# Kernel optimization log

Hardware: AMD Instinct MI355X
Metric: run time of the kernel (lower is better)

## Reference

```python
import jax, jax.numpy as jnp
import numpy as np

EMBED_DIM = 768
NUM_HEADS = 12
HEAD_DIM = EMBED_DIM // NUM_HEADS


def setup_inputs() -> dict:
    key = jax.random.key(0)
    ks = jax.random.split(key, 9)
    B, N, D = 8, 1024, EMBED_DIM
    s = 1.0 / np.sqrt(D)
    x = jax.random.normal(ks[0], (B, N, D), dtype=jnp.float32)
    Wq = jax.random.normal(ks[1], (D, D), dtype=jnp.float32) * s
    bq = jnp.zeros((D,), dtype=jnp.float32)
    Wk = jax.random.normal(ks[2], (D, D), dtype=jnp.float32) * s
    bk = jnp.zeros((D,), dtype=jnp.float32)
    Wv = jax.random.normal(ks[3], (D, D), dtype=jnp.float32) * s
    bv = jnp.zeros((D,), dtype=jnp.float32)
    Wo = jax.random.normal(ks[4], (D, D), dtype=jnp.float32) * s
    bo = jnp.zeros((D,), dtype=jnp.float32)
    return {"x": x, "Wq": Wq, "bq": bq, "Wk": Wk, "bk": bk,
            "Wv": Wv, "bv": bv, "Wo": Wo, "bo": bo}


def reference(x, Wq, bq, Wk, bk, Wv, bv, Wo, bo):
    B, N, D = x.shape
    H, Hd = NUM_HEADS, HEAD_DIM
    # torch Linear: y = x @ W.T + b
    q = (x @ Wq.T + bq).reshape(B, N, H, Hd).transpose(0, 2, 1, 3)  # [B,H,N,Hd]
    k = (x @ Wk.T + bk).reshape(B, N, H, Hd).transpose(0, 2, 1, 3)
    v = (x @ Wv.T + bv).reshape(B, N, H, Hd).transpose(0, 2, 1, 3)
    # NOTE: original scales by embed_dim**-0.5 (not head_dim)
    scale = jnp.asarray(D, x.dtype) ** -0.5
    scores = jnp.einsum('bhnd,bhmd->bhnm', q, k) * scale  # [B,H,N,N]
    attn = jax.nn.softmax(scores, axis=-1)
    out = jnp.einsum('bhnm,bhmd->bhnd', attn, v)  # dropout: identity in eval
    out = out.transpose(0, 2, 1, 3).reshape(B, N, D)
    return out @ Wo.T + bo
```

## Files before the change

### kernel.cpp

```cpp
#include <hip/hip_runtime.h>
#include <math.h>


typedef __bf16 bf16x8 __attribute__((ext_vector_type(8)));
typedef float  f32x4  __attribute__((ext_vector_type(4)));
typedef unsigned u32x2 __attribute__((ext_vector_type(2)));
typedef unsigned u32x4 __attribute__((ext_vector_type(4)));
typedef unsigned short ushort_t;

__device__ __forceinline__ unsigned short f2bf(float f) {
    unsigned u = __float_as_uint(f);
    u += 0x7fffu + ((u >> 16) & 1u);
    return (unsigned short)(u >> 16);
}
__device__ __forceinline__ unsigned pk16(unsigned short lo, unsigned short hi) {
    return (unsigned)lo | ((unsigned)hi << 16);
}

#define GLL16(g, l)                                                                        \
    __builtin_amdgcn_global_load_lds((const __attribute__((address_space(1))) void*)(g),   \
                                     (__attribute__((address_space(3))) void*)(l), 16, 0, 0)

__global__ __launch_bounds__(256)
void cast_all(const float* __restrict__ x,
              const float* __restrict__ w0, const float* __restrict__ w1,
              const float* __restrict__ w2, const float* __restrict__ w3,
              ushort_t* __restrict__ xb, ushort_t* __restrict__ wb0,
              ushort_t* __restrict__ wb1, ushort_t* __restrict__ wb2,
              ushort_t* __restrict__ wb3)
{
    const int y = blockIdx.y;
    const float* s; ushort_t* d; int n;
    switch (y) {
        case 0:  s = x;  d = xb;  n = 8192 * 768; break;
        case 1:  s = w0; d = wb0; n = 768 * 768;  break;
        case 2:  s = w1; d = wb1; n = 768 * 768;  break;
        case 3:  s = w2; d = wb2; n = 768 * 768;  break;
        default: s = w3; d = wb3; n = 768 * 768;  break;
    }
    const int i = (blockIdx.x * 256 + threadIdx.x) * 8;
    if (i >= n) return;
    const float4 f0 = *(const float4*)(s + i);
    const float4 f1 = *(const float4*)(s + i + 4);
    ushort4 p0, p1;
    p0.x = f2bf(f0.x); p0.y = f2bf(f0.y); p0.z = f2bf(f0.z); p0.w = f2bf(f0.w);
    p1.x = f2bf(f1.x); p1.y = f2bf(f1.y); p1.z = f2bf(f1.z); p1.w = f2bf(f1.w);
    *(ushort4*)(d + i)     = p0;
    *(ushort4*)(d + i + 4) = p1;
}

__device__ __forceinline__ void gemm_core_mfma(
    const ushort_t* __restrict__ A, const ushort_t* __restrict__ W,
    int m0, int n0, ushort_t* smem, f32x4 acc[4][4])
{
    ushort_t* As = smem;
    ushort_t* Ws = smem + 4096;
    const int tid = threadIdx.x;
    const int L   = tid & 63;
    const int wv  = tid >> 6;
    const int wr  = wv >> 1, wc = wv & 1;
    const int c   = L & 15,  g  = L >> 4;

    const int c0 = tid, c1 = tid + 256;
    const int qs = ((tid & 3) ^ ((tid >> 3) & 3)) * 8;
    const ushort_t* a0 = A + (size_t)(m0 + (c0 >> 2)) * 768 + qs;
    const ushort_t* a1 = A + (size_t)(m0 + (c1 >> 2)) * 768 + qs;
    const ushort_t* w0 = W + (size_t)(n0 + (c0 >> 2)) * 768 + qs;
    const ushort_t* w1 = W + (size_t)(n0 + (c1 >> 2)) * 768 + qs;
    const int sg = (g ^ ((c >> 1) & 3)) * 8;

#pragma unroll
    for (int i = 0; i < 4; ++i)
#pragma unroll
        for (int j = 0; j < 4; ++j) acc[i][j] = (f32x4){0.f, 0.f, 0.f, 0.f};

    for (int k0 = 0; k0 < 768; k0 += 32) {
        __syncthreads();
        GLL16(a0 + k0, &As[(size_t)c0 * 8]);
        GLL16(a1 + k0, &As[(size_t)c1 * 8]);
        GLL16(w0 + k0, &Ws[(size_t)c0 * 8]);
        GLL16(w1 + k0, &Ws[(size_t)c1 * 8]);
        __syncthreads();
        bf16x8 af[4], bfr[4];
#pragma unroll
        for (int i = 0; i < 4; ++i)
            af[i] = *(const bf16x8*)&As[(wr * 64 + i * 16 + c) * 32 + sg];
#pragma unroll
        for (int j = 0; j < 4; ++j)
            bfr[j] = *(const bf16x8*)&Ws[(wc * 64 + j * 16 + c) * 32 + sg];
#pragma unroll
        for (int i = 0; i < 4; ++i)
#pragma unroll
            for (int j = 0; j < 4; ++j)
                acc[i][j] = __builtin_amdgcn_mfma_f32_16x16x32_bf16(
                    af[i], bfr[j], acc[i][j], 0, 0, 0);
    }
}

__global__ __launch_bounds__(256, 3)
void gemm_qkv(const ushort_t* __restrict__ xb,
              const ushort_t* __restrict__ wqb, const ushort_t* __restrict__ wkb,
              const ushort_t* __restrict__ wvb,
              const float* __restrict__ bq, const float* __restrict__ bk,
              const float* __restrict__ bv,
              ushort_t* __restrict__ Qh, ushort_t* __restrict__ Kl,
              ushort_t* __restrict__ Vl)
{
    __shared__ ushort_t smem[8192];
    const int z = blockIdx.z;
    const ushort_t* W   = (z == 0) ? wqb : (z == 1) ? wkb : wvb;
    const float*    bia = (z == 0) ? bq  : (z == 1) ? bk  : bv;
    const int m0 = blockIdx.y * 128, n0 = blockIdx.x * 128;
    f32x4 acc[4][4];
    gemm_core_mfma(xb, W, m0, n0, smem, acc);

    const int tid = threadIdx.x, L = tid & 63, wv2 = tid >> 6;
    const int wr = wv2 >> 1, wc = wv2 & 1, c = L & 15, g = L >> 4;
    ushort_t* scr = smem + wv2 * 1280;
    const int h = (n0 + wc * 64) >> 6;
    float bsv[4];
#pragma unroll
    for (int j = 0; j < 4; ++j) bsv[j] = bia[n0 + wc * 64 + j * 16 + c];

    __syncthreads();
#pragma unroll
    for (int i = 0; i < 4; ++i) {
        const int rowg = m0 + wr * 64 + i * 16;
        const int b  = rowg >> 10;
        const int nb = rowg & 1023;
        const int bh = b * 12 + h;
        if (z < 2) {
#pragma unroll
            for (int j = 0; j < 4; ++j)
#pragma unroll
                for (int r = 0; r < 4; ++r)
                    scr[(g * 4 + r) * 72 + j * 16 + c] = f2bf(acc[i][j][r] + bsv[j]);
            if (z == 0) {
                const int row = L >> 2, qp = L & 3;
                const u32x4 v0 = *(const u32x4*)&scr[row * 72 + qp * 16];
                const u32x4 v1 = *(const u32x4*)&scr[row * 72 + qp * 16 + 8];
                ushort_t* dst = Qh + ((size_t)bh * 1024 + nb + row) * 64 + qp * 16;
                *(u32x4*)dst       = v0;
                *(u32x4*)(dst + 8) = v1;
            } else {
                const int n16 = L >> 2, q1 = L & 3;
                const u32x4 va  = *(const u32x4*)&scr[n16 * 72 + q1 * 8];
                const u32x4 vb2 = *(const u32x4*)&scr[n16 * 72 + q1 * 8 + 32];
                ushort_t* base = Kl + (size_t)bh * 65536 + (size_t)(nb >> 4) * 1024;
                *(u32x4*)&base[q1 * 128 + n16 * 8]       = va;
                *(u32x4*)&base[512 + q1 * 128 + n16 * 8] = vb2;
            }
        } else {
#pragma unroll
            for (int j = 0; j < 4; ++j) {
                const unsigned w01 = pk16(f2bf(acc[i][j][0] + bsv[j]),
                                          f2bf(acc[i][j][1] + bsv[j]));
                const unsigned w23 = pk16(f2bf(acc[i][j][2] + bsv[j]),
                                          f2bf(acc[i][j][3] + bsv[j]));
                const int a = (j * 16 + c) * 20 + g * 4;
                *(unsigned*)&scr[a]     = w01;
                *(unsigned*)&scr[a + 2] = w23;
            }
            const u32x2 r0 = *(const u32x2*)&scr[L * 20];
            const u32x2 r1 = *(const u32x2*)&scr[L * 20 + 4];
            const u32x2 r2 = *(const u32x2*)&scr[L * 20 + 8];
            const u32x2 r3 = *(const u32x2*)&scr[L * 20 + 12];
            const int ht = L >> 4, cV = L & 15;
            const int T = nb >> 6, u = (nb >> 5) & 1, gVa = (nb >> 3) & 3;
            ushort_t* vb = Vl + (((size_t)(bh * 4 + ht) * 16 + T) * 2 + u) * 512 + cV * 8;
            *(u32x4*)&vb[gVa * 128]       = (u32x4){r0.x, r0.y, r1.x, r1.y};
            *(u32x4*)&vb[(gVa + 1) * 128] = (u32x4){r2.x, r2.y, r3.x, r3.y};
        }
    }
}

__global__ __launch_bounds__(256, 3)
void gemm_outp(const ushort_t* __restrict__ attnb, const ushort_t* __restrict__ wob,
               const float* __restrict__ bo, float* __restrict__ out)
{
    __shared__ ushort_t smem[8192];
    const int m0 = blockIdx.y * 128, n0 = blockIdx.x * 128;
    f32x4 acc[4][4];
    gemm_core_mfma(attnb, wob, m0, n0, smem, acc);
    const int tid = threadIdx.x, L = tid & 63, wv2 = tid >> 6;
    const int wr = wv2 >> 1, wc = wv2 & 1, c = L & 15, g = L >> 4;
#pragma unroll
    for (int i = 0; i < 4; ++i) {
        const int row = m0 + wr * 64 + i * 16 + g * 4;
#pragma unroll
        for (int j = 0; j < 4; ++j) {
            const int col = n0 + wc * 64 + j * 16 + c;
            const float bsvo = bo[col];
#pragma unroll
            for (int r = 0; r < 4; ++r)
                out[(size_t)(row + r) * 768 + col] = acc[i][j][r] + bsvo;
        }
    }
}

__global__ __launch_bounds__(64, 3)
void flash_bf16(const ushort_t* __restrict__ Q, const ushort_t* __restrict__ Kl,
                const ushort_t* __restrict__ Vl, ushort_t* __restrict__ attnb)
{
    __shared__ ushort_t Ps[2][16 * 68];
    const int L = threadIdx.x;
    const int c = L & 15, g = L >> 4;
    const int bh = blockIdx.x, q0 = blockIdx.y * 32;
    const float SC2 = 0.05205954985329743f;

    const ushort_t* Qp = Q + ((size_t)bh * 1024 + q0 + c) * 64 + g * 8;
    bf16x8 qf[2][2];
    qf[0][0] = *(const bf16x8*)Qp;
    qf[0][1] = *(const bf16x8*)(Qp + 32);
    qf[1][0] = *(const bf16x8*)(Qp + 16 * 64);
    qf[1][1] = *(const bf16x8*)(Qp + 16 * 64 + 32);

    const ushort_t* Kb = Kl + (size_t)bh * 65536 + (size_t)L * 8;
    const ushort_t* Vb = Vl + (size_t)bh * 65536 + (size_t)L * 8;

    f32x4 o[2][4];
#pragma unroll
    for (int w = 0; w < 2; ++w)
#pragma unroll
        for (int ht = 0; ht < 4; ++ht) o[w][ht] = (f32x4){0.f, 0.f, 0.f, 0.f};
    float ls[2] = {0.f, 0.f};

    bf16x8 kf0[4], kf1[4];
#pragma unroll
    for (int ct = 0; ct < 4; ++ct) {
        kf0[ct] = *(const bf16x8*)(Kb + (size_t)(ct * 2 + 0) * 512);
        kf1[ct] = *(const bf16x8*)(Kb + (size_t)(ct * 2 + 1) * 512);
    }

    for (int T = 0; T < 16; ++T) {
        bf16x8 vf0[4], vf1[4];
#pragma unroll
        for (int ht = 0; ht < 4; ++ht) {
            const ushort_t* vp = Vb + (size_t)((ht * 16 + T) * 2) * 512;
            vf0[ht] = *(const bf16x8*)vp;
            vf1[ht] = *(const bf16x8*)(vp + 512);
        }
        f32x4 s[2][4];
#pragma unroll
        for (int w = 0; w < 2; ++w)
#pragma unroll
            for (int ct = 0; ct < 4; ++ct) {
                f32x4 zz = (f32x4){0.f, 0.f, 0.f, 0.f};
                zz = __builtin_amdgcn_mfma_f32_16x16x32_bf16(kf0[ct], qf[w][0], zz, 0, 0, 0);
                zz = __builtin_amdgcn_mfma_f32_16x16x32_bf16(kf1[ct], qf[w][1], zz, 0, 0, 0);
                s[w][ct] = zz;
            }
        const int Tn = (T < 15) ? T + 1 : 15;
#pragma unroll
        for (int ct = 0; ct < 4; ++ct) {
            const ushort_t* kp = Kb + (size_t)((Tn * 4 + ct) * 2) * 512;
            kf0[ct] = *(const bf16x8*)kp;
            kf1[ct] = *(const bf16x8*)(kp + 512);
        }
#pragma unroll
        for (int w = 0; w < 2; ++w) {
#pragma unroll
            for (int ct = 0; ct < 4; ++ct) {
                float p[4];
#pragma unroll
                for (int r = 0; r < 4; ++r)
                    p[r] = __builtin_amdgcn_exp2f(s[w][ct][r] * SC2);
                ls[w] += (p[0] + p[1]) + (p[2] + p[3]);
                const unsigned w01 = __builtin_amdgcn_perm(
                    __float_as_uint(p[1]), __float_as_uint(p[0]), 0x07060302u);
                const unsigned w23 = __builtin_amdgcn_perm(
                    __float_as_uint(p[3]), __float_as_uint(p[2]), 0x07060302u);
                *(u32x2*)&Ps[w][c * 68 + ct * 16 + g * 4] = (u32x2){w01, w23};
            }
        }
#pragma unroll
        for (int w = 0; w < 2; ++w) {
            const int pb = c * 68 + g * 8;
            const u32x4 pa  = *(const u32x4*)&Ps[w][pb];
            const u32x4 pbv = *(const u32x4*)&Ps[w][pb + 32];
            const bf16x8 pf0 = __builtin_bit_cast(bf16x8, pa);
            const bf16x8 pf1 = __builtin_bit_cast(bf16x8, pbv);
#pragma unroll
            for (int ht = 0; ht < 4; ++ht) {
                o[w][ht] = __builtin_amdgcn_mfma_f32_16x16x32_bf16(vf0[ht], pf0, o[w][ht], 0, 0, 0);
                o[w][ht] = __builtin_amdgcn_mfma_f32_16x16x32_bf16(vf1[ht], pf1, o[w][ht], 0, 0, 0);
            }
        }
    }

    const int b = bh / 12, h = bh % 12;
#pragma unroll
    for (int w = 0; w < 2; ++w) {
        float l = ls[w];
        l += __shfl_xor(l, 16);
        l += __shfl_xor(l, 32);
        const float inv = 1.f / l;
#pragma unroll
        for (int ht = 0; ht < 4; ++ht) {
            const unsigned w0 = pk16(f2bf(o[w][ht][0] * inv), f2bf(o[w][ht][1] * inv));
            const unsigned w1 = pk16(f2bf(o[w][ht][2] * inv), f2bf(o[w][ht][3] * inv));
            *(u32x2*)&Ps[w][c * 68 + ht * 16 + g * 4] = (u32x2){w0, w1};
        }
#pragma unroll
        for (int e = 0; e < 2; ++e) {
            const int row = e * 8 + (L >> 3);
            const int ch  = L & 7;
            const int si  = row * 68 + ch * 8;
            const u32x2 t0 = *(const u32x2*)&Ps[w][si];
            const u32x2 t1 = *(const u32x2*)&Ps[w][si + 4];
            *(u32x4*)&attnb[((size_t)(b * 1024 + q0 + w * 16 + row)) * 768 + h * 64 + ch * 8]
                = (u32x4){t0.x, t0.y, t1.x, t1.y};
        }
    }
}

extern "C" void kernel_launch(void* const* d_in, const int* in_sizes, int n_in,
                              void* d_out, int out_size, void* d_ws, size_t ws_size,
                              hipStream_t stream)
{
    const float* x  = (const float*)d_in[0];
    const float* Wq = (const float*)d_in[1];
    const float* bq = (const float*)d_in[2];
    const float* Wk = (const float*)d_in[3];
    const float* bk = (const float*)d_in[4];
    const float* Wv = (const float*)d_in[5];
    const float* bv = (const float*)d_in[6];
    const float* Wo = (const float*)d_in[7];
    const float* bo = (const float*)d_in[8];
    float* out = (float*)d_out;

    char* ws = (char*)d_ws;
    ushort_t* xb    = (ushort_t*)(ws);
    ushort_t* wqb   = (ushort_t*)(ws + 12582912);
    ushort_t* wkb   = (ushort_t*)(ws + 12582912 + 1179648);
    ushort_t* wvb   = (ushort_t*)(ws + 12582912 + 2359296);
    ushort_t* wob   = (ushort_t*)(ws + 12582912 + 3538944);
    ushort_t* Qh    = (ushort_t*)(ws + 17301504);
    ushort_t* Kl    = (ushort_t*)(ws + 29884416);
    ushort_t* Vl    = (ushort_t*)(ws + 42467328);
    ushort_t* attnb = (ushort_t*)(ws + 55050240);

    cast_all<<<dim3(3072, 5), 256, 0, stream>>>(x, Wq, Wk, Wv, Wo,
                                                xb, wqb, wkb, wvb, wob);
    gemm_qkv<<<dim3(6, 64, 3), 256, 0, stream>>>(xb, wqb, wkb, wvb,
                                                 bq, bk, bv, Qh, Kl, Vl);
    flash_bf16<<<dim3(96, 32), 64, 0, stream>>>(Qh, Kl, Vl, attnb);
    gemm_outp<<<dim3(6, 64), 256, 0, stream>>>(attnb, wob, bo, out);
}
```

Before: 198.7 us.

## Fuse Q/K/V projections into one GEMM sharing the x tile across three weights

The QKV projection previously launched a separate grid slice per weight matrix, each reloading the same x tile. It now computes all three projections in one block on a 64x128 tile. The block loads x once per k-step alongside three weight tiles and keeps three accumulator sets. Epilogues are rewritten per output layout for Q, K and V. This cuts redundant x traffic and LDS loads, at the cost of more registers per thread and smaller M tiles, which may reduce occupancy.

```diff
diff --git a/kernel.cpp b/kernel.cpp
--- a/kernel.cpp
+++ b/kernel.cpp
@@ -106,71 +106,125 @@
               ushort_t* __restrict__ Qh, ushort_t* __restrict__ Kl,
               ushort_t* __restrict__ Vl)
 {
-    __shared__ ushort_t smem[8192];
-    const int z = blockIdx.z;
-    const ushort_t* W   = (z == 0) ? wqb : (z == 1) ? wkb : wvb;
-    const float*    bia = (z == 0) ? bq  : (z == 1) ? bk  : bv;
-    const int m0 = blockIdx.y * 128, n0 = blockIdx.x * 128;
-    f32x4 acc[4][4];
-    gemm_core_mfma(xb, W, m0, n0, smem, acc);
-
-    const int tid = threadIdx.x, L = tid & 63, wv2 = tid >> 6;
-    const int wr = wv2 >> 1, wc = wv2 & 1, c = L & 15, g = L >> 4;
-    ushort_t* scr = smem + wv2 * 1280;
-    const int h = (n0 + wc * 64) >> 6;
-    float bsv[4];
-#pragma unroll
-    for (int j = 0; j < 4; ++j) bsv[j] = bia[n0 + wc * 64 + j * 16 + c];
+    __shared__ ushort_t smem[14336];
+    ushort_t* As  = smem;
+    ushort_t* Ws0 = smem + 2048;
+    ushort_t* Ws1 = smem + 6144;
+    ushort_t* Ws2 = smem + 10240;
+
+    const int tid = threadIdx.x, L = tid & 63, wv = tid >> 6;
+    const int c = L & 15, g = L >> 4;
+    const int n0 = blockIdx.x * 128, m0 = blockIdx.y * 64;
+
+    const int qs = ((tid & 3) ^ ((tid >> 3) & 3)) * 8;
+    const ushort_t* ap = xb  + (size_t)(m0 + (tid >> 2)) * 768 + qs;
+    const ushort_t* wq = wqb + (size_t)(n0 + (tid >> 2)) * 768 + qs;
+    const ushort_t* wk = wkb + (size_t)(n0 + (tid >> 2)) * 768 + qs;
+    const ushort_t* wvp = wvb + (size_t)(n0 + (tid >> 2)) * 768 + qs;
+    const size_t st64 = (size_t)64 * 768;
+    const int sg = (g ^ ((c >> 1) & 3)) * 8;
+
+    f32x4 acc[3][4][2];
+#pragma unroll
+    for (int z = 0; z < 3; ++z)
+#pragma unroll
+        for (int i = 0; i < 4; ++i)
+#pragma unroll
+            for (int j = 0; j < 2; ++j) acc[z][i][j] = (f32x4){0.f, 0.f, 0.f, 0.f};
+
+    for (int k0 = 0; k0 < 768; k0 += 32) {
+        __syncthreads();
+        GLL16(ap + k0,          &As[(size_t)tid * 8]);
+        GLL16(wq + k0,          &Ws0[(size_t)tid * 8]);
+        GLL16(wq + st64 + k0,   &Ws0[(size_t)(tid + 256) * 8]);
+        GLL16(wk + k0,          &Ws1[(size_t)tid * 8]);
+        GLL16(wk + st64 + k0,   &Ws1[(size_t)(tid + 256) * 8]);
+        GLL16(wvp + k0,         &Ws2[(size_t)tid * 8]);
+        GLL16(wvp + st64 + k0,  &Ws2[(size_t)(tid + 256) * 8]);
+        __syncthreads();
+        bf16x8 af[4];
+#pragma unroll
+        for (int i = 0; i < 4; ++i)
+            af[i] = *(const bf16x8*)&As[(i * 16 + c) * 32 + sg];
+        bf16x8 bf[3][2];
+        const ushort_t* wsz[3] = {Ws0, Ws1, Ws2};
+#pragma unroll
+        for (int z = 0; z < 3; ++z)
+#pragma unroll
+            for (int j = 0; j < 2; ++j)
+                bf[z][j] = *(const bf16x8*)&wsz[z][(wv * 32 + j * 16 + c) * 32 + sg];
+#pragma unroll
+        for (int z = 0; z < 3; ++z)
+#pragma unroll
+            for (int i = 0; i < 4; ++i)
+#pragma unroll
+                for (int j = 0; j < 2; ++j)
+                    acc[z][i][j] = __builtin_amdgcn_mfma_f32_16x16x32_bf16(
+                        af[i], bf[z][j], acc[z][i][j], 0, 0, 0);
+    }
+
+    const int b  = m0 >> 10, nb = m0 & 1023;
+    const int hcol = n0 + wv * 32;
+    const int h = hcol >> 6, uh = (hcol >> 5) & 1;
+    const int bh = b * 12 + h;
+    ushort_t* scr = smem + wv * 2304;
+
+    float bias2[3][2];
+#pragma unroll
+    for (int j = 0; j < 2; ++j) {
+        bias2[0][j] = bq[hcol + j * 16 + c];
+        bias2[1][j] = bk[hcol + j * 16 + c];
+        bias2[2][j] = bv[hcol + j * 16 + c];
+    }
 
     __syncthreads();
-#pragma unroll
-    for (int i = 0; i < 4; ++i) {
-        const int rowg = m0 + wr * 64 + i * 16;
-        const int b  = rowg >> 10;
-        const int nb = rowg & 1023;
-        const int bh = b * 12 + h;
-        if (z < 2) {
-#pragma unroll
-            for (int j = 0; j < 4; ++j)
-#pragma unroll
-                for (int r = 0; r < 4; ++r)
-                    scr[(g * 4 + r) * 72 + j * 16 + c] = f2bf(acc[i][j][r] + bsv[j]);
-            if (z == 0) {
-                const int row = L >> 2, qp = L & 3;
-                const u32x4 v0 = *(const u32x4*)&scr[row * 72 + qp * 16];
-                const u32x4 v1 = *(const u32x4*)&scr[row * 72 + qp * 16 + 8];
-                ushort_t* dst = Qh + ((size_t)bh * 1024 + nb + row) * 64 + qp * 16;
-                *(u32x4*)dst       = v0;
-                *(u32x4*)(dst + 8) = v1;
-            } else {
-                const int n16 = L >> 2, q1 = L & 3;
-                const u32x4 va  = *(const u32x4*)&scr[n16 * 72 + q1 * 8];
-                const u32x4 vb2 = *(const u32x4*)&scr[n16 * 72 + q1 * 8 + 32];
-                ushort_t* base = Kl + (size_t)bh * 65536 + (size_t)(nb >> 4) * 1024;
-                *(u32x4*)&base[q1 * 128 + n16 * 8]       = va;
-                *(u32x4*)&base[512 + q1 * 128 + n16 * 8] = vb2;
-            }
-        } else {
-#pragma unroll
-            for (int j = 0; j < 4; ++j) {
-                const unsigned w01 = pk16(f2bf(acc[i][j][0] + bsv[j]),
-                                          f2bf(acc[i][j][1] + bsv[j]));
-                const unsigned w23 = pk16(f2bf(acc[i][j][2] + bsv[j]),
-                                          f2bf(acc[i][j][3] + bsv[j]));
-                const int a = (j * 16 + c) * 20 + g * 4;
-                *(unsigned*)&scr[a]     = w01;
-                *(unsigned*)&scr[a + 2] = w23;
-            }
-            const u32x2 r0 = *(const u32x2*)&scr[L * 20];
-            const u32x2 r1 = *(const u32x2*)&scr[L * 20 + 4];
-            const u32x2 r2 = *(const u32x2*)&scr[L * 20 + 8];
-            const u32x2 r3 = *(const u32x2*)&scr[L * 20 + 12];
-            const int ht = L >> 4, cV = L & 15;
-            const int T = nb >> 6, u = (nb >> 5) & 1, gVa = (nb >> 3) & 3;
-            ushort_t* vb = Vl + (((size_t)(bh * 4 + ht) * 16 + T) * 2 + u) * 512 + cV * 8;
-            *(u32x4*)&vb[gVa * 128]       = (u32x4){r0.x, r0.y, r1.x, r1.y};
-            *(u32x4*)&vb[(gVa + 1) * 128] = (u32x4){r2.x, r2.y, r3.x, r3.y};
-        }
+
+#pragma unroll
+    for (int i = 0; i < 4; ++i)
+#pragma unroll
+        for (int j = 0; j < 2; ++j)
+#pragma unroll
+            for (int r = 0; r < 4; ++r)
+                scr[(i * 16 + g * 4 + r) * 36 + j * 16 + c] =
+                    f2bf(acc[0][i][j][r] + bias2[0][j]);
+#pragma unroll
+    for (int e = 0; e < 4; ++e) {
+        const int slot = e * 64 + L;
+        const int row = slot >> 2, ch = slot & 3;
+        const u32x4 v = *(const u32x4*)&scr[row * 36 + ch * 8];
+        *(u32x4*)&Qh[((size_t)bh * 1024 + nb + row) * 64 + uh * 32 + ch * 8] = v;
+    }
+
+#pragma unroll
+    for (int i = 0; i < 4; ++i)
+#pragma unroll
+        for (int j = 0; j < 2; ++j)
+#pragma unroll
+            for (int r = 0; r < 4; ++r)
+                scr[(i * 16 + g * 4 + r) * 36 + j * 16 + c] =
+                    f2bf(acc[1][i][j][r] + bias2[1][j]);
+#pragma unroll
+    for (int tau = 0; tau < 4; ++tau) {
+        const u32x4 v = *(const u32x4*)&scr[(tau * 16 + c) * 36 + g * 8];
+        *(u32x4*)&Kl[(((size_t)bh * 64 + (nb >> 4) + tau) * 2 + uh) * 512
+                     + (size_t)L * 8] = v;
+    }
+
+#pragma unroll
+    for (int i = 0; i < 4; ++i)
+#pragma unroll
+        for (int j = 0; j < 2; ++j)
+#pragma unroll
+            for (int r = 0; r < 4; ++r)
+                scr[(j * 16 + c) * 68 + i * 16 + g * 4 + r] =
+                    f2bf(acc[2][i][j][r] + bias2[2][j]);
+    const int T = nb >> 6;
+#pragma unroll
+    for (int t = 0; t < 4; ++t) {
+        const int htl = t >> 1, u = t & 1;
+        const u32x4 v = *(const u32x4*)&scr[(htl * 16 + c) * 68 + u * 32 + g * 8];
+        *(u32x4*)&Vl[((((size_t)bh * 4 + uh * 2 + htl) * 16 + T) * 2 + u) * 512
+                     + (size_t)L * 8] = v;
     }
 }
 
@@ -342,8 +396,8 @@
 
     cast_all<<<dim3(3072, 5), 256, 0, stream>>>(x, Wq, Wk, Wv, Wo,
                                                 xb, wqb, wkb, wvb, wob);
-    gemm_qkv<<<dim3(6, 64, 3), 256, 0, stream>>>(xb, wqb, wkb, wvb,
-                                                 bq, bk, bv, Qh, Kl, Vl);
+    gemm_qkv<<<dim3(6, 128), 256, 0, stream>>>(xb, wqb, wkb, wvb,
+                                               bq, bk, bv, Qh, Kl, Vl);
     flash_bf16<<<dim3(96, 32), 64, 0, stream>>>(Qh, Kl, Vl, attnb);
     gemm_outp<<<dim3(6, 64), 256, 0, stream>>>(attnb, wob, bo, out);
 }
```

New measurement: 196.4 us. About the same (-1.2%).
